# Kernel optimization log

Hardware: AMD Instinct MI355X
Metric: run time of the kernel (lower is better)

Reference implementation:

```python
import jax, jax.numpy as jnp
import numpy as np

EPS = 1e-6
K = 1.0          # curvature parameter from init_kwargs
DIM = 2          # spatial dim hardcoded via default dim=2 in log/exponential
N = 500_000      # num vertices
E = 8_000_000    # num edges
M = 8            # message feature dim


def setup_inputs() -> dict:
    key = jax.random.key(0)
    k1, k2, k3, k4 = jax.random.split(key, 4)
    # vertices on hyperboloid: -x0^2 + |xs|^2 = -K  =>  x0 = sqrt(K + |xs|^2)
    xs = jax.random.normal(k1, (N, DIM), jnp.float32) * 0.5
    x0 = jnp.sqrt(K + jnp.sum(xs * xs, -1, keepdims=True))
    vertices = jnp.concatenate([x0, xs], -1)                      # [N, 3]
    src = jax.random.randint(k2, (E,), 0, N)
    off = jax.random.randint(k3, (E,), 1, N)                      # avoid self-loops
    dst = (src + off) % N
    edges = jnp.stack([src, dst], -1)                             # [E, 2] int
    messages = jax.random.normal(k4, (E, M), jnp.float32)         # [E, M]
    return {"vertices": vertices, "edges": edges, "messages": messages}


def _mip(x, y, w):
    # Minkowski inner product, keepdims=True: [.., 3] -> [.., 1]
    return jnp.sum(x * y * w, -1, keepdims=True)


def reference(vertices, edges, messages):
    w = jnp.concatenate([-jnp.ones(1), jnp.ones(DIM)]).astype(vertices.dtype)
    weights = jnp.mean(messages, -1, keepdims=True)               # [E, 1]
    x = vertices[edges[:, 0]]                                     # [E, 3] source
    y = vertices[edges[:, 1]]                                     # [E, 3] target
    # log map: log_x(y)
    t = _mip(x, y, w)                                             # [E, 1]
    v = y + x * t / K
    vnorm = jnp.sqrt(_mip(v, v, w) + EPS)
    dist = jnp.arccosh(-t / K)                                    # hyperboloid distance
    vectors = (v / vnorm) * dist * weights                        # [E, 3]
    # unsorted_segment_mean over source vertex (empty segments -> 0, as in TF)
    seg = edges[:, 0]
    sums = jax.ops.segment_sum(vectors, seg, num_segments=N)      # [N, 3]
    cnt = jax.ops.segment_sum(jnp.ones((E, 1), vertices.dtype), seg, num_segments=N)
    agg = jnp.where(cnt > 0, sums / jnp.maximum(cnt, 1.0), 0.0)   # [N, 3]
    # exponential map exp_vertices(agg)
    anorm = jnp.sqrt(_mip(agg, agg, w) + EPS)
    sqrtk = np.float32(np.sqrt(K))
    T = anorm / sqrtk
    return jnp.cosh(T) * vertices + sqrtk * jnp.sinh(T) * (agg / anorm)
```

## Files before the change

### kernel.cpp

```cpp
#include <hip/hip_runtime.h>

#define EPSF 1e-6f
#define VB 4096
#define VB_SHIFT 12
#define CHUNK 4096
#define NBMAX 128
#define NSLICE 2


__global__ __launch_bounds__(512) void count_kernel(const int2* __restrict__ edges,
                                                    int* __restrict__ counts,
                                                    int E, int nb)
{
    __shared__ int hist[NBMAX];
    int c = blockIdx.x;
    int base = c * CHUNK;
    int cnt = min(CHUNK, E - base);
    for (int i = threadIdx.x; i < nb; i += 512) hist[i] = 0;
    __syncthreads();
    for (int k = threadIdx.x; k < cnt; k += 512) {
        int src = edges[base + k].x;
        atomicAdd(&hist[src >> VB_SHIFT], 1);
    }
    __syncthreads();
    for (int i = threadIdx.x; i < nb; i += 512) counts[(size_t)c * nb + i] = hist[i];
}

__global__ __launch_bounds__(64) void relscan_kernel(int* __restrict__ counts,
                                                     int* __restrict__ totals,
                                                     int nb, int nchunk)
{
    int b = blockIdx.x;
    int lane = threadIdx.x;
    int running = 0;
    for (int cbase = 0; cbase < nchunk; cbase += 64) {
        int c = cbase + lane;
        int v = (c < nchunk) ? counts[(size_t)c * nb + b] : 0;
        int s = v;
        for (int d = 1; d < 64; d <<= 1) {
            int o = __shfl_up(s, d);
            if (lane >= d) s += o;
        }
        if (c < nchunk) counts[(size_t)c * nb + b] = running + (s - v);
        running += __shfl(s, 63);
    }
    if (lane == 0) totals[b] = running;
}

__global__ __launch_bounds__(64) void bstart_kernel(const int* __restrict__ totals,
                                                    int* __restrict__ bucketStart, int nb)
{
    if (threadIdx.x == 0 && blockIdx.x == 0) {
        int run = 0;
        for (int b = 0; b < nb; ++b) { bucketStart[b] = run; run += totals[b]; }
        bucketStart[nb] = run;
    }
}

__global__ __launch_bounds__(512) void scatter_kernel(const int2* __restrict__ edges,
    const float4* __restrict__ messages,
    const int* __restrict__ rel,
    const int* __restrict__ bucketStart,
    unsigned int* __restrict__ bsd,
    float* __restrict__ bw,
    int E, int nb)
{
    __shared__ unsigned int  s_pack[CHUNK];
    __shared__ float         s_w[CHUNK];
    __shared__ unsigned char s_b[CHUNK];
    __shared__ int hist[NBMAX], lstart[NBMAX], cursor[NBMAX], goff[NBMAX];

    int c = blockIdx.x;
    int base = c * CHUNK;
    int cnt = min(CHUNK, E - base);

    for (int i = threadIdx.x; i < nb; i += 512) hist[i] = 0;
    __syncthreads();

    int2 ed[8]; float wg[8];
#pragma unroll
    for (int j = 0; j < 8; ++j) {
        int k = threadIdx.x + j * 512;
        if (k < cnt) {
            int2 e2 = edges[base + k];
            float4 m0 = messages[2 * (size_t)(base + k)];
            float4 m1 = messages[2 * (size_t)(base + k) + 1];
            ed[j] = e2;
            wg[j] = (((m0.x + m0.y) + (m0.z + m0.w)) +
                     ((m1.x + m1.y) + (m1.z + m1.w))) * 0.125f;
            atomicAdd(&hist[e2.x >> VB_SHIFT], 1);
        }
    }
    __syncthreads();
    if (threadIdx.x == 0) {
        int run = 0;
        for (int b = 0; b < nb; ++b) { lstart[b] = run; cursor[b] = run; run += hist[b]; }
    }
    __syncthreads();
#pragma unroll
    for (int j = 0; j < 8; ++j) {
        int k = threadIdx.x + j * 512;
        if (k < cnt) {
            int b = ed[j].x >> VB_SHIFT;
            int pos = atomicAdd(&cursor[b], 1);
            s_pack[pos] = ((unsigned int)(ed[j].x & (VB - 1)) << 19) | (unsigned int)ed[j].y;
            s_w[pos]    = wg[j];
            s_b[pos]    = (unsigned char)b;
        }
    }
    for (int i = threadIdx.x; i < nb; i += 512)
        goff[i] = bucketStart[i] + rel[(size_t)c * nb + i];
    __syncthreads();
    for (int k = threadIdx.x; k < cnt; k += 512) {
        int b = s_b[k];
        int g = goff[b] + (k - lstart[b]);
        bsd[g] = s_pack[k];
        bw[g]  = s_w[k];
    }
}

__global__ __launch_bounds__(1024) void accum_kernel(const float* __restrict__ vertices,
    const unsigned int* __restrict__ bsd, const float* __restrict__ bw,
    const int* __restrict__ bucketStart,
    float* __restrict__ partial,
    int N, int nb)
{
    __shared__ float acc[4][VB];
    int b = blockIdx.x / NSLICE;
    int s = blockIdx.x - b * NSLICE;
    for (int i = threadIdx.x; i < VB; i += 1024) {
        acc[0][i] = 0.f; acc[1][i] = 0.f; acc[2][i] = 0.f; acc[3][i] = 0.f;
    }
    __syncthreads();
    int e0 = bucketStart[b], e1 = bucketStart[b + 1];
    int len = e1 - e0;
    int g0 = e0 + (int)((long long)len * s / NSLICE);
    int g1 = e0 + (int)((long long)len * (s + 1) / NSLICE);
    int vbase = b << VB_SHIFT;
    for (int g = g0 + threadIdx.x; g < g1; g += 1024) {
        unsigned int pack = bsd[g];
        float w = bw[g];
        int dst = (int)(pack & 0x7FFFFu);
        int sl  = (int)(pack >> 19);
        const float* xp = vertices + 3 * (size_t)(vbase + sl);
        const float* yp = vertices + 3 * (size_t)dst;
        float x0 = xp[0], x1 = xp[1], x2 = xp[2];
        float y0 = yp[0], y1 = yp[1], y2 = yp[2];
        float t  = x1 * y1 + x2 * y2 - x0 * y0;
        float v0 = y0 + x0 * t;
        float v1 = y1 + x1 * t;
        float v2 = y2 + x2 * t;
        float vn = sqrtf(v1 * v1 + v2 * v2 - v0 * v0 + EPSF);
        float scale = acoshf(-t) * w / vn;
        atomicAdd(&acc[0][sl], v0 * scale);
        atomicAdd(&acc[1][sl], v1 * scale);
        atomicAdd(&acc[2][sl], v2 * scale);
        atomicAdd(&acc[3][sl], 1.0f);
    }
    __syncthreads();
    float* pb = partial + (size_t)s * 4 * N;
    for (int i = threadIdx.x; i < VB; i += 1024) {
        int v = vbase + i;
        if (v < N) {
            pb[v]                 = acc[0][i];
            pb[(size_t)N + v]     = acc[1][i];
            pb[2 * (size_t)N + v] = acc[2][i];
            pb[3 * (size_t)N + v] = acc[3][i];
        }
    }
}

__global__ __launch_bounds__(256) void final_kernel(const float* __restrict__ vertices,
    const float* __restrict__ partial, float* __restrict__ out, int N)
{
    int i = blockIdx.x * 256 + threadIdx.x;
    if (i >= N) return;
    float s0 = 0.f, s1 = 0.f, s2 = 0.f, sc = 0.f;
#pragma unroll
    for (int s = 0; s < NSLICE; ++s) {
        const float* pb = partial + (size_t)s * 4 * N;
        s0 += pb[i];
        s1 += pb[(size_t)N + i];
        s2 += pb[2 * (size_t)N + i];
        sc += pb[3 * (size_t)N + i];
    }
    float g0 = 0.f, g1 = 0.f, g2 = 0.f;
    if (sc > 0.f) { g0 = s0 / sc; g1 = s1 / sc; g2 = s2 / sc; }
    float an = sqrtf(g1 * g1 + g2 * g2 - g0 * g0 + EPSF);
    float ch = coshf(an);
    float sh = sinhf(an) / an;
    size_t bix = 3 * (size_t)i;
    out[bix + 0] = ch * vertices[bix + 0] + sh * g0;
    out[bix + 1] = ch * vertices[bix + 1] + sh * g1;
    out[bix + 2] = ch * vertices[bix + 2] + sh * g2;
}


__global__ __launch_bounds__(256) void zero_kernel(float4* __restrict__ acc, int n4)
{
    int stride = gridDim.x * blockDim.x;
    for (int i = blockIdx.x * blockDim.x + threadIdx.x; i < n4; i += stride)
        acc[i] = make_float4(0.f, 0.f, 0.f, 0.f);
}

__global__ __launch_bounds__(256) void edge_kernel_dev(const float* __restrict__ vertices,
    const int2* __restrict__ edges, const float4* __restrict__ messages,
    float* __restrict__ acc, int E)
{
    int stride = gridDim.x * blockDim.x;
    for (int e = blockIdx.x * blockDim.x + threadIdx.x; e < E; e += stride) {
        int2 ed = edges[e];
        float4 m0 = messages[2 * e];
        float4 m1 = messages[2 * e + 1];
        float wgt = (((m0.x + m0.y) + (m0.z + m0.w)) +
                     ((m1.x + m1.y) + (m1.z + m1.w))) * 0.125f;
        const float* xp = vertices + 3 * (size_t)ed.x;
        const float* yp = vertices + 3 * (size_t)ed.y;
        float x0 = xp[0], x1 = xp[1], x2 = xp[2];
        float y0 = yp[0], y1 = yp[1], y2 = yp[2];
        float t  = x1 * y1 + x2 * y2 - x0 * y0;
        float v0 = y0 + x0 * t;
        float v1 = y1 + x1 * t;
        float v2 = y2 + x2 * t;
        float vn = sqrtf(v1 * v1 + v2 * v2 - v0 * v0 + EPSF);
        float scale = acoshf(-t) * wgt / vn;
        float* a = acc + 4 * (size_t)ed.x;
        atomicAdd(a + 0, v0 * scale);
        atomicAdd(a + 1, v1 * scale);
        atomicAdd(a + 2, v2 * scale);
        atomicAdd(a + 3, 1.0f);
    }
}

__global__ __launch_bounds__(256) void vertex_kernel_fb(const float* __restrict__ vertices,
    const float4* __restrict__ acc, float* __restrict__ out, int N)
{
    int i = blockIdx.x * blockDim.x + threadIdx.x;
    if (i >= N) return;
    float4 a = acc[i];
    float g0 = 0.f, g1 = 0.f, g2 = 0.f;
    if (a.w > 0.f) { g0 = a.x / a.w; g1 = a.y / a.w; g2 = a.z / a.w; }
    float an = sqrtf(g1 * g1 + g2 * g2 - g0 * g0 + EPSF);
    float ch = coshf(an);
    float sh = sinhf(an) / an;
    size_t bix = 3 * (size_t)i;
    out[bix + 0] = ch * vertices[bix + 0] + sh * g0;
    out[bix + 1] = ch * vertices[bix + 1] + sh * g1;
    out[bix + 2] = ch * vertices[bix + 2] + sh * g2;
}


extern "C" void kernel_launch(void* const* d_in, const int* in_sizes, int n_in,
                              void* d_out, int out_size, void* d_ws, size_t ws_size,
                              hipStream_t stream)
{
    const float*  vertices = (const float*)d_in[0];
    const int2*   edges    = (const int2*)d_in[1];
    const float4* messages = (const float4*)d_in[2];
    float* out = (float*)d_out;

    int N = in_sizes[0] / 3;
    int E = in_sizes[1] / 2;
    int nb = (N + VB - 1) / VB;
    int nchunk = (E + CHUNK - 1) / CHUNK;

    size_t off = 0;
    auto alloc = [&](size_t bytes) { size_t o = off; off = (off + bytes + 255) & ~255ull; return o; };
    size_t o_bsd = alloc((size_t)E * 4);
    size_t o_bw  = alloc((size_t)E * 4);
    size_t o_cnt = alloc((size_t)nchunk * nb * 4);
    size_t o_tot = alloc((size_t)nb * 4);
    size_t o_bst = alloc((size_t)(nb + 1) * 4);
    size_t o_par = alloc((size_t)NSLICE * 4 * (size_t)N * 4);
    size_t need = off;

    if (nb <= NBMAX && (unsigned)N <= (1u << 19) && ws_size >= need) {
        char* w = (char*)d_ws;
        unsigned int* bsd = (unsigned int*)(w + o_bsd);
        float* bw         = (float*)(w + o_bw);
        int* counts       = (int*)(w + o_cnt);
        int* totals       = (int*)(w + o_tot);
        int* bstart       = (int*)(w + o_bst);
        float* partial    = (float*)(w + o_par);

        count_kernel<<<nchunk, 512, 0, stream>>>(edges, counts, E, nb);
        relscan_kernel<<<nb, 64, 0, stream>>>(counts, totals, nb, nchunk);
        bstart_kernel<<<1, 64, 0, stream>>>(totals, bstart, nb);
        scatter_kernel<<<nchunk, 512, 0, stream>>>(edges, messages, counts, bstart,
                                                   bsd, bw, E, nb);
        accum_kernel<<<nb * NSLICE, 1024, 0, stream>>>(vertices, bsd, bw, bstart,
                                                       partial, N, nb);
        final_kernel<<<(N + 255) / 256, 256, 0, stream>>>(vertices, partial, out, N);
    } else {
        float* acc = (float*)d_ws;
        zero_kernel<<<4096, 256, 0, stream>>>((float4*)acc, N);
        edge_kernel_dev<<<4096, 256, 0, stream>>>(vertices, edges, messages, acc, E);
        vertex_kernel_fb<<<(N + 255) / 256, 256, 0, stream>>>(vertices, (const float4*)acc, out, N);
    }
}
```

Baseline: 304.3 us.

## Pad vertices to float4, interleave edge records, shrink buckets and add slices

```diff
diff --git a/kernel.cpp b/kernel.cpp
--- a/kernel.cpp
+++ b/kernel.cpp
@@ -1,12 +1,20 @@
 #include <hip/hip_runtime.h>
 
 #define EPSF 1e-6f
-#define VB 4096
-#define VB_SHIFT 12
+#define VB 2048
+#define VB_SHIFT 11
 #define CHUNK 4096
-#define NBMAX 128
-#define NSLICE 2
-
+#define NBMAX 256
+
+__global__ __launch_bounds__(256) void pad_kernel(const float* __restrict__ v,
+                                                  float4* __restrict__ v4, int N)
+{
+    int stride = gridDim.x * blockDim.x;
+    for (int i = blockIdx.x * blockDim.x + threadIdx.x; i < N; i += stride) {
+        size_t b = 3 * (size_t)i;
+        v4[i] = make_float4(v[b], v[b + 1], v[b + 2], 0.f);
+    }
+}
 
 __global__ __launch_bounds__(512) void count_kernel(const int2* __restrict__ edges,
                                                     int* __restrict__ counts,
@@ -61,8 +69,7 @@
     const float4* __restrict__ messages,
     const int* __restrict__ rel,
     const int* __restrict__ bucketStart,
-    unsigned int* __restrict__ bsd,
-    float* __restrict__ bw,
+    uint2* __restrict__ rec,
     int E, int nb)
 {
     __shared__ unsigned int  s_pack[CHUNK];
@@ -114,38 +121,48 @@
     for (int k = threadIdx.x; k < cnt; k += 512) {
         int b = s_b[k];
         int g = goff[b] + (k - lstart[b]);
-        bsd[g] = s_pack[k];
-        bw[g]  = s_w[k];
-    }
-}
-
-__global__ __launch_bounds__(1024) void accum_kernel(const float* __restrict__ vertices,
-    const unsigned int* __restrict__ bsd, const float* __restrict__ bw,
+        rec[g] = make_uint2(s_pack[k], __float_as_uint(s_w[k]));
+    }
+}
+
+template <bool USEV4>
+__global__ __launch_bounds__(512) void accum_kernel(
+    const float4* __restrict__ vert4,
+    const float*  __restrict__ verts,
+    const uint2*  __restrict__ rec,
     const int* __restrict__ bucketStart,
     float* __restrict__ partial,
-    int N, int nb)
+    int N, int nslice)
 {
     __shared__ float acc[4][VB];
-    int b = blockIdx.x / NSLICE;
-    int s = blockIdx.x - b * NSLICE;
-    for (int i = threadIdx.x; i < VB; i += 1024) {
+    int b = blockIdx.x / nslice;
+    int s = blockIdx.x - b * nslice;
+    for (int i = threadIdx.x; i < VB; i += 512) {
         acc[0][i] = 0.f; acc[1][i] = 0.f; acc[2][i] = 0.f; acc[3][i] = 0.f;
     }
     __syncthreads();
     int e0 = bucketStart[b], e1 = bucketStart[b + 1];
     int len = e1 - e0;
-    int g0 = e0 + (int)((long long)len * s / NSLICE);
-    int g1 = e0 + (int)((long long)len * (s + 1) / NSLICE);
+    int g0 = e0 + (int)((long long)len * s / nslice);
+    int g1 = e0 + (int)((long long)len * (s + 1) / nslice);
     int vbase = b << VB_SHIFT;
-    for (int g = g0 + threadIdx.x; g < g1; g += 1024) {
-        unsigned int pack = bsd[g];
-        float w = bw[g];
-        int dst = (int)(pack & 0x7FFFFu);
-        int sl  = (int)(pack >> 19);
-        const float* xp = vertices + 3 * (size_t)(vbase + sl);
-        const float* yp = vertices + 3 * (size_t)dst;
-        float x0 = xp[0], x1 = xp[1], x2 = xp[2];
-        float y0 = yp[0], y1 = yp[1], y2 = yp[2];
+    for (int g = g0 + threadIdx.x; g < g1; g += 512) {
+        uint2 r = rec[g];
+        float w = __uint_as_float(r.y);
+        int dst = (int)(r.x & 0x7FFFFu);
+        int sl  = (int)(r.x >> 19);
+        float x0, x1, x2, y0, y1, y2;
+        if (USEV4) {
+            float4 xv = vert4[vbase + sl];
+            float4 yv = vert4[dst];
+            x0 = xv.x; x1 = xv.y; x2 = xv.z;
+            y0 = yv.x; y1 = yv.y; y2 = yv.z;
+        } else {
+            const float* xp = verts + 3 * (size_t)(vbase + sl);
+            const float* yp = verts + 3 * (size_t)dst;
+            x0 = xp[0]; x1 = xp[1]; x2 = xp[2];
+            y0 = yp[0]; y1 = yp[1]; y2 = yp[2];
+        }
         float t  = x1 * y1 + x2 * y2 - x0 * y0;
         float v0 = y0 + x0 * t;
         float v1 = y1 + x1 * t;
@@ -159,7 +176,7 @@
     }
     __syncthreads();
     float* pb = partial + (size_t)s * 4 * N;
-    for (int i = threadIdx.x; i < VB; i += 1024) {
+    for (int i = threadIdx.x; i < VB; i += 512) {
         int v = vbase + i;
         if (v < N) {
             pb[v]                 = acc[0][i];
@@ -171,13 +188,12 @@
 }
 
 __global__ __launch_bounds__(256) void final_kernel(const float* __restrict__ vertices,
-    const float* __restrict__ partial, float* __restrict__ out, int N)
+    const float* __restrict__ partial, float* __restrict__ out, int N, int nslice)
 {
     int i = blockIdx.x * 256 + threadIdx.x;
     if (i >= N) return;
     float s0 = 0.f, s1 = 0.f, s2 = 0.f, sc = 0.f;
-#pragma unroll
-    for (int s = 0; s < NSLICE; ++s) {
+    for (int s = 0; s < nslice; ++s) {
         const float* pb = partial + (size_t)s * 4 * N;
         s0 += pb[i];
         s1 += pb[(size_t)N + i];
@@ -266,31 +282,45 @@
 
     size_t off = 0;
     auto alloc = [&](size_t bytes) { size_t o = off; off = (off + bytes + 255) & ~255ull; return o; };
-    size_t o_bsd = alloc((size_t)E * 4);
-    size_t o_bw  = alloc((size_t)E * 4);
+    size_t o_rec = alloc((size_t)E * 8);
     size_t o_cnt = alloc((size_t)nchunk * nb * 4);
     size_t o_tot = alloc((size_t)nb * 4);
     size_t o_bst = alloc((size_t)(nb + 1) * 4);
-    size_t o_par = alloc((size_t)NSLICE * 4 * (size_t)N * 4);
-    size_t need = off;
-
-    if (nb <= NBMAX && (unsigned)N <= (1u << 19) && ws_size >= need) {
+    size_t fixed = off;
+
+    size_t par_bytes = 4ull * (size_t)N * 4;
+    size_t v4_bytes  = (size_t)N * 16;
+
+    int nslice = 0; bool usev4 = false;
+    if (fixed + v4_bytes + 4 * par_bytes <= ws_size)      { nslice = 4; usev4 = true; }
+    else if (fixed + v4_bytes + 2 * par_bytes <= ws_size) { nslice = 2; usev4 = true; }
+    else if (fixed + 2 * par_bytes <= ws_size)            { nslice = 2; usev4 = false; }
+
+    if (nb <= NBMAX && (unsigned)N <= (1u << 19) && nslice > 0) {
         char* w = (char*)d_ws;
-        unsigned int* bsd = (unsigned int*)(w + o_bsd);
-        float* bw         = (float*)(w + o_bw);
-        int* counts       = (int*)(w + o_cnt);
-        int* totals       = (int*)(w + o_tot);
-        int* bstart       = (int*)(w + o_bst);
-        float* partial    = (float*)(w + o_par);
-
+        uint2* rec   = (uint2*)(w + o_rec);
+        int* counts  = (int*)(w + o_cnt);
+        int* totals  = (int*)(w + o_tot);
+        int* bstart  = (int*)(w + o_bst);
+        size_t o2 = fixed;
+        float4* v4 = nullptr;
+        if (usev4) { v4 = (float4*)(w + o2); o2 += (v4_bytes + 255) & ~255ull; }
+        float* partial = (float*)(w + o2);
+
+        if (usev4)
+            pad_kernel<<<1024, 256, 0, stream>>>(vertices, v4, N);
         count_kernel<<<nchunk, 512, 0, stream>>>(edges, counts, E, nb);
         relscan_kernel<<<nb, 64, 0, stream>>>(counts, totals, nb, nchunk);
         bstart_kernel<<<1, 64, 0, stream>>>(totals, bstart, nb);
         scatter_kernel<<<nchunk, 512, 0, stream>>>(edges, messages, counts, bstart,
-                                                   bsd, bw, E, nb);
-        accum_kernel<<<nb * NSLICE, 1024, 0, stream>>>(vertices, bsd, bw, bstart,
-                                                       partial, N, nb);
-        final_kernel<<<(N + 255) / 256, 256, 0, stream>>>(vertices, partial, out, N);
+                                                   rec, E, nb);
+        if (usev4)
+            accum_kernel<true><<<nb * nslice, 512, 0, stream>>>(v4, vertices, rec, bstart,
+                                                                partial, N, nslice);
+        else
+            accum_kernel<false><<<nb * nslice, 512, 0, stream>>>(nullptr, vertices, rec, bstart,
+                                                                 partial, N, nslice);
+        final_kernel<<<(N + 255) / 256, 256, 0, stream>>>(vertices, partial, out, N, nslice);
     } else {
         float* acc = (float*)d_ws;
         zero_kernel<<<4096, 256, 0, stream>>>((float4*)acc, N);
```

New measurement: 322.2 us. +5.9%, slower.
